# Performance work log

Hardware: AMD Instinct MI355X
Metric: run time of the kernel (lower is better)

## Reference

```python
import jax, jax.numpy as jnp
import numpy as np

CHUNK = 32  # chunk_size in _delta_rule_chunkwise

def _l2norm(x, eps=1e-6):
    return x * jax.lax.rsqrt(jnp.sum(x * x, axis=-1, keepdims=True) + eps)

def setup_inputs() -> dict:
    key = jax.random.key(0)
    kq, kk, kv, kb = jax.random.split(key, 4)
    b, h, L, dk, dv = 2, 8, 4096, 128, 128
    return {
        "q": jax.random.normal(kq, (b, h, L, dk), jnp.float32),
        "k": jax.random.normal(kk, (b, h, L, dk), jnp.float32),
        "v": jax.random.normal(kv, (b, h, L, dv), jnp.float32),
        "beta": jax.random.uniform(kb, (b, h, L), jnp.float32),  # sigmoid(b_proj) in (0,1)
    }

def _delta_rule_chunkwise(q, k, v, beta, chunk_size=CHUNK):
    b, h, L, dk = q.shape
    dv = v.shape[-1]
    c = chunk_size
    pad = (-L) % c
    if pad:
        q = jnp.pad(q, ((0, 0), (0, 0), (0, pad), (0, 0)))
        k = jnp.pad(k, ((0, 0), (0, 0), (0, pad), (0, 0)))
        v = jnp.pad(v, ((0, 0), (0, 0), (0, pad), (0, 0)))
        beta = jnp.pad(beta, ((0, 0), (0, 0), (0, pad)))
    n = (L + pad) // c
    q = _l2norm(q)
    k = _l2norm(k)
    v = v * beta[..., None]
    k_beta = k * beta[..., None]
    # [b,h,n,c,d]
    resh = lambda t: t.reshape(b, h, n, c, t.shape[-1])
    q, k, v, k_beta = map(resh, (q, k, v, k_beta))
    # strictly-lower-triangular -(k_beta k^T)
    lower = jnp.tril(jnp.ones((c, c), bool), -1)
    att = -(k_beta @ jnp.swapaxes(k, -1, -2)) * lower
    # forward substitution: invert (I - A) for strictly lower A (unrolled, c=32 static)
    for i in range(1, c):
        upd = jnp.einsum('...j,...jm->...m', att[..., i, :], att[..., :, :i])
        att = att.at[..., i, :i].add(upd)
    att = att + jnp.eye(c, dtype=att.dtype)
    att = att.astype(jnp.bfloat16).astype(q.dtype)  # matches .to(torch.bfloat16)
    u = att @ v         # [b,h,n,c,dv]
    w = att @ k_beta    # [b,h,n,c,dk]
    future = jnp.triu(jnp.ones((c, c), bool), 1)
    S0 = jnp.zeros((b, h, dk, dv), q.dtype)

    def step(S, inp):
        q_i, k_i, u_i, w_i = inp  # [b,h,c,d]
        att_local = jnp.where(future, 0.0, q_i @ jnp.swapaxes(k_i, -1, -2))
        u_new = u_i - w_i @ S
        o_i = q_i @ S + att_local @ u_new
        S_new = S + jnp.swapaxes(k_i, -1, -2) @ u_new
        return S_new, o_i

    xs = tuple(jnp.moveaxis(t, 2, 0) for t in (q, k, u, w))  # scan over chunks
    S, o = jax.lax.scan(step, S0, xs)
    o = jnp.moveaxis(o, 0, 2).reshape(b, h, n * c, dv)[:, :, :L]
    return o, S

def reference(q, k, v, beta):
    return _delta_rule_chunkwise(q, k, v, beta)
```

## Files before the change

kernel.cpp:

```cpp
#include <hip/hip_runtime.h>
#include <hip/hip_bf16.h>


#define B 2
#define H 8
#define LSEQ 4096
#define DK 128
#define DV 128
#define C 32
#define NCHUNK (LSEQ / C)
#define BH (B * H)
#define NBLK (BH * NCHUNK)
#define NG 16
#define GSZ 8

typedef _Float16 f16x8 __attribute__((ext_vector_type(8)));
typedef float f32x4 __attribute__((ext_vector_type(4)));

union U4H8 { uint4 u; f16x8 h; };

__device__ inline unsigned short f2h(float f) {
    _Float16 h = (_Float16)f;
    unsigned short u;
    __builtin_memcpy(&u, &h, 2);
    return u;
}
__device__ inline float h2f(unsigned int v) {
    unsigned short s = (unsigned short)v;
    _Float16 h;
    __builtin_memcpy(&h, &s, 2);
    return (float)h;
}
__device__ inline unsigned int pack2(float a, float b) {
    return (unsigned int)f2h(a) | ((unsigned int)f2h(b) << 16);
}
__device__ inline float dot4(float4 a, float4 b) {
    return a.x * b.x + a.y * b.y + a.z * b.z + a.w * b.w;
}
__device__ inline float bf16r(float x) {
    return __bfloat162float(__float2bfloat16(x));
}
__device__ inline uint2 pk4(float v0, float v1, float v2, float v3) {
    uint2 p; p.x = pack2(v0, v1); p.y = pack2(v2, v3); return p;
}
__device__ inline f32x4 up4(uint2 p) {
    f32x4 v;
    v[0] = h2f(p.x & 0xffffu); v[1] = h2f(p.x >> 16);
    v[2] = h2f(p.y & 0xffffu); v[3] = h2f(p.y >> 16);
    return v;
}

#define S40 40
#define S136 136

__global__ __launch_bounds__(64) void phase2_kernel(
    const float* __restrict__ qg, const float* __restrict__ kg,
    const float* __restrict__ vg, const float* __restrict__ betag,
    uint4* __restrict__ wnegf, uint4* __restrict__ qnf,
    uint4* __restrict__ ktf, uint4* __restrict__ atf,
    uint2* __restrict__ uf)
{
    __shared__ alignas(16) _Float16 sA [32 * S40];
    __shared__ alignas(16) _Float16 sAT[32 * S40];
    __shared__ alignas(16) _Float16 sTT[32 * S40];
    __shared__ alignas(16) _Float16 sTB[32 * S40];
    __shared__ alignas(16) _Float16 sW [32 * S136];
    __shared__ alignas(16) float sbetaL[32];
    __shared__ alignas(16) float skscL[32];

    const int l = threadIdx.x;
    const int lm = l & 15, qd = l >> 4;
    const int blk = blockIdx.x;
    const long tb = (long)blk * C * DK;
    const f32x4 z4 = {0.f, 0.f, 0.f, 0.f};

    if (l < 32) sbetaL[l] = betag[(long)blk * C + l];

    U4H8 qF[8], kF[8];
    float ssq[2] = {0.f, 0.f}, ssk[2] = {0.f, 0.f};
    #pragma unroll
    for (int mt = 0; mt < 2; mt++) {
        #pragma unroll
        for (int kt = 0; kt < 4; kt++) {
            const float* qp = qg + tb + (long)(mt * 16 + lm) * DK + kt * 32 + qd * 8;
            const float* kp = kg + tb + (long)(mt * 16 + lm) * DK + kt * 32 + qd * 8;
            float4 a0 = *(const float4*)qp, a1 = *(const float4*)(qp + 4);
            float4 b0 = *(const float4*)kp, b1 = *(const float4*)(kp + 4);
            ssq[mt] += dot4(a0, a0) + dot4(a1, a1);
            ssk[mt] += dot4(b0, b0) + dot4(b1, b1);
            U4H8 x;
            x.u.x = pack2(a0.x, a0.y); x.u.y = pack2(a0.z, a0.w);
            x.u.z = pack2(a1.x, a1.y); x.u.w = pack2(a1.z, a1.w);
            qF[mt * 4 + kt] = x;
            U4H8 y;
            y.u.x = pack2(b0.x, b0.y); y.u.y = pack2(b0.z, b0.w);
            y.u.z = pack2(b1.x, b1.y); y.u.w = pack2(b1.z, b1.w);
            kF[mt * 4 + kt] = y;
        }
    }
    float qsc[2], ksc[2];
    #pragma unroll
    for (int mt = 0; mt < 2; mt++) {
        float s = ssq[mt];
        s += __shfl_xor(s, 16, 64);
        s += __shfl_xor(s, 32, 64);
        qsc[mt] = rsqrtf(s + 1e-6f);
        float t = ssk[mt];
        t += __shfl_xor(t, 16, 64);
        t += __shfl_xor(t, 32, 64);
        ksc[mt] = rsqrtf(t + 1e-6f);
    }
    if (qd == 0) { skscL[lm] = ksc[0]; skscL[16 + lm] = ksc[1]; }

    f32x4 alT[3] = {z4, z4, z4};
    #pragma unroll
    for (int kt = 0; kt < 4; kt++) {
        alT[0] = __builtin_amdgcn_mfma_f32_16x16x32_f16(kF[kt].h,     qF[kt].h,     alT[0], 0, 0, 0);
        alT[1] = __builtin_amdgcn_mfma_f32_16x16x32_f16(kF[kt].h,     qF[4 + kt].h, alT[1], 0, 0, 0);
        alT[2] = __builtin_amdgcn_mfma_f32_16x16x32_f16(kF[4 + kt].h, qF[4 + kt].h, alT[2], 0, 0, 0);
    }
    #pragma unroll
    for (int mt = 0; mt < 2; mt++) {
        _Float16 qs = (_Float16)qsc[mt];
        #pragma unroll
        for (int kt = 0; kt < 4; kt++) {
            U4H8 x;
            x.h = qF[mt * 4 + kt].h * qs;
            qnf[((long)blk * 8 + mt * 4 + kt) * 64 + l] = x.u;
        }
    }
    f32x4 rw[4] = {z4, z4, z4, z4};
    #pragma unroll
    for (int kt = 0; kt < 4; kt++) {
        rw[0] = __builtin_amdgcn_mfma_f32_16x16x32_f16(kF[kt].h,     kF[kt].h,     rw[0], 0, 0, 0);
        rw[1] = __builtin_amdgcn_mfma_f32_16x16x32_f16(kF[kt].h,     kF[4 + kt].h, rw[1], 0, 0, 0);
        rw[2] = __builtin_amdgcn_mfma_f32_16x16x32_f16(kF[4 + kt].h, kF[kt].h,     rw[2], 0, 0, 0);
        rw[3] = __builtin_amdgcn_mfma_f32_16x16x32_f16(kF[4 + kt].h, kF[4 + kt].h, rw[3], 0, 0, 0);
    }

    float4 b4[2], ks4[2];
    b4[0]  = *(const float4*)&sbetaL[qd * 4];      b4[1]  = *(const float4*)&sbetaL[16 + qd * 4];
    ks4[0] = *(const float4*)&skscL[qd * 4];       ks4[1] = *(const float4*)&skscL[16 + qd * 4];
    const float bcol0 = sbetaL[lm], bcol1 = sbetaL[16 + lm];

    {
        *(uint2*)&sTB[lm * S40 + 16 + qd * 4] = (uint2){0u, 0u};
        float v[4];
        #pragma unroll
        for (int r = 0; r < 4; r++) {
            int c = qd * 4 + r;
            v[r] = (c <= lm) ? (qsc[0] * (&ks4[0].x)[r] * alT[0][r]) : 0.f;
        }
        *(uint2*)&sTB[lm * S40 + qd * 4] = pk4(v[0], v[1], v[2], v[3]);
        #pragma unroll
        for (int r = 0; r < 4; r++) v[r] = qsc[1] * (&ks4[0].x)[r] * alT[1][r];
        *(uint2*)&sTB[(16 + lm) * S40 + qd * 4] = pk4(v[0], v[1], v[2], v[3]);
        #pragma unroll
        for (int r = 0; r < 4; r++) {
            int c = qd * 4 + r;
            v[r] = (c <= lm) ? (qsc[1] * (&ks4[1].x)[r] * alT[2][r]) : 0.f;
        }
        *(uint2*)&sTB[(16 + lm) * S40 + 16 + qd * 4] = pk4(v[0], v[1], v[2], v[3]);
    }
    #pragma unroll
    for (int f = 0; f < 2; f++) {
        uint4 x = *(const uint4*)&sTB[(f * 16 + lm) * S40 + qd * 8];
        atf[((long)blk * 2 + f) * 64 + l] = x;
    }

    {
        float v[4];
        *(uint2*)&sA [lm * S40 + 16 + qd * 4]        = (uint2){0u, 0u};
        *(uint2*)&sAT[(16 + lm) * S40 + qd * 4]      = (uint2){0u, 0u};
        *(uint2*)&sTT[(16 + lm) * S40 + qd * 4]      = (uint2){0u, 0u};
        #pragma unroll
        for (int r = 0; r < 4; r++) {
            int c = qd * 4 + r;
            v[r] = (c < lm) ? (-bcol0 * ksc[0] * (&ks4[0].x)[r] * rw[0][r]) : 0.f;
        }
        *(uint2*)&sA[lm * S40 + qd * 4] = pk4(v[0], v[1], v[2], v[3]);
        #pragma unroll
        for (int r = 0; r < 4; r++) v[r] = -bcol1 * ksc[1] * (&ks4[0].x)[r] * rw[1][r];
        *(uint2*)&sA[(16 + lm) * S40 + qd * 4] = pk4(v[0], v[1], v[2], v[3]);
        #pragma unroll
        for (int r = 0; r < 4; r++) {
            int c = qd * 4 + r;
            v[r] = (c < lm) ? (-bcol1 * ksc[1] * (&ks4[1].x)[r] * rw[3][r]) : 0.f;
        }
        *(uint2*)&sA[(16 + lm) * S40 + 16 + qd * 4] = pk4(v[0], v[1], v[2], v[3]);
        #pragma unroll
        for (int r = 0; r < 4; r++) {
            int c = qd * 4 + r;
            v[r] = (c > lm) ? (-(&b4[0].x)[r] * (&ks4[0].x)[r] * ksc[0] * rw[0][r]) : 0.f;
        }
        *(uint2*)&sAT[lm * S40 + qd * 4] = pk4(v[0], v[1], v[2], v[3]);
        #pragma unroll
        for (int r = 0; r < 4; r++) v[r] = -(&b4[1].x)[r] * (&ks4[1].x)[r] * ksc[0] * rw[2][r];
        *(uint2*)&sAT[lm * S40 + 16 + qd * 4] = pk4(v[0], v[1], v[2], v[3]);
        #pragma unroll
        for (int r = 0; r < 4; r++) {
            int c = qd * 4 + r;
            v[r] = (c > lm) ? (-(&b4[1].x)[r] * (&ks4[1].x)[r] * ksc[1] * rw[3][r]) : 0.f;
        }
        *(uint2*)&sAT[(16 + lm) * S40 + 16 + qd * 4] = pk4(v[0], v[1], v[2], v[3]);
        #pragma unroll
        for (int r = 0; r < 4; r++) {
            int c = qd * 4 + r;
            v[r] = (c > lm) ? (-(&b4[0].x)[r] * (&ks4[0].x)[r] * ksc[0] * rw[0][r])
                            : ((c == lm) ? 1.0f : 0.f);
        }
        *(uint2*)&sTT[lm * S40 + qd * 4] = pk4(v[0], v[1], v[2], v[3]);
        #pragma unroll
        for (int r = 0; r < 4; r++) v[r] = -(&b4[1].x)[r] * (&ks4[1].x)[r] * ksc[0] * rw[2][r];
        *(uint2*)&sTT[lm * S40 + 16 + qd * 4] = pk4(v[0], v[1], v[2], v[3]);
        #pragma unroll
        for (int r = 0; r < 4; r++) {
            int c = qd * 4 + r;
            v[r] = (c > lm) ? (-(&b4[1].x)[r] * (&ks4[1].x)[r] * ksc[1] * rw[3][r])
                            : ((c == lm) ? 1.0f : 0.f);
        }
        *(uint2*)&sTT[(16 + lm) * S40 + 16 + qd * 4] = pk4(v[0], v[1], v[2], v[3]);
    }
    f32x4 Tc[3], TTc[3];
    #pragma unroll
    for (int r = 0; r < 4; r++) {
        int rr = qd * 4 + r;
        Tc[0][r] = (lm < rr) ? (-(&b4[0].x)[r] * (&ks4[0].x)[r] * ksc[0] * rw[0][r])
                             : ((lm == rr) ? 1.0f : 0.f);
        Tc[1][r] = -(&b4[1].x)[r] * (&ks4[1].x)[r] * ksc[0] * rw[2][r];
        Tc[2][r] = (lm < rr) ? (-(&b4[1].x)[r] * (&ks4[1].x)[r] * ksc[1] * rw[3][r])
                             : ((lm == rr) ? 1.0f : 0.f);
        TTc[0][r] = (rr < lm) ? (-bcol0 * ksc[0] * (&ks4[0].x)[r] * rw[0][r])
                              : ((rr == lm) ? 1.0f : 0.f);
        TTc[1][r] = -bcol1 * ksc[1] * (&ks4[0].x)[r] * rw[1][r];
        TTc[2][r] = (rr < lm) ? (-bcol1 * ksc[1] * (&ks4[1].x)[r] * rw[3][r])
                              : ((rr == lm) ? 1.0f : 0.f);
    }

    #pragma unroll
    for (int p = 0; p < 4; p++) {
        U4H8 AF[2], ATF[2], TTF[2];
        AF[0].u  = *(const uint4*)&sA [lm * S40 + qd * 8];
        AF[1].u  = *(const uint4*)&sA [(16 + lm) * S40 + qd * 8];
        ATF[0].u = *(const uint4*)&sAT[lm * S40 + qd * 8];
        ATF[1].u = *(const uint4*)&sAT[(16 + lm) * S40 + qd * 8];
        TTF[0].u = *(const uint4*)&sTT[lm * S40 + qd * 8];
        TTF[1].u = *(const uint4*)&sTT[(16 + lm) * S40 + qd * 8];

        f32x4 A2_00 = __builtin_amdgcn_mfma_f32_16x16x32_f16(AF[0].h, ATF[0].h, z4, 0, 0, 0);
        f32x4 A2_10 = __builtin_amdgcn_mfma_f32_16x16x32_f16(AF[1].h, ATF[0].h, z4, 0, 0, 0);
        f32x4 A2_11 = __builtin_amdgcn_mfma_f32_16x16x32_f16(AF[1].h, ATF[1].h, z4, 0, 0, 0);
        f32x4 A2T_00 = __builtin_amdgcn_mfma_f32_16x16x32_f16(ATF[0].h, AF[0].h, z4, 0, 0, 0);
        f32x4 A2T_01 = __builtin_amdgcn_mfma_f32_16x16x32_f16(ATF[0].h, AF[1].h, z4, 0, 0, 0);
        f32x4 A2T_11 = __builtin_amdgcn_mfma_f32_16x16x32_f16(ATF[1].h, AF[1].h, z4, 0, 0, 0);

        {
            float v[4];
            #pragma unroll
            for (int r = 0; r < 4; r++) { int c = qd * 4 + r; v[r] = (c < lm) ? A2T_00[r] : 0.f; }
            *(uint2*)&sA[lm * S40 + qd * 4] = pk4(v[0], v[1], v[2], v[3]);
            *(uint2*)&sA[(16 + lm) * S40 + qd * 4] = pk4(A2T_01[0], A2T_01[1], A2T_01[2], A2T_01[3]);
            #pragma unroll
            for (int r = 0; r < 4; r++) { int c = qd * 4 + r; v[r] = (c < lm) ? A2T_11[r] : 0.f; }
            *(uint2*)&sA[(16 + lm) * S40 + 16 + qd * 4] = pk4(v[0], v[1], v[2], v[3]);
        }
        if (p < 3) {
            float v[4];
            #pragma unroll
            for (int r = 0; r < 4; r++) { int c = qd * 4 + r; v[r] = (c > lm) ? A2_00[r] : 0.f; }
            *(uint2*)&sAT[lm * S40 + qd * 4] = pk4(v[0], v[1], v[2], v[3]);
            *(uint2*)&sAT[lm * S40 + 16 + qd * 4] = pk4(A2_10[0], A2_10[1], A2_10[2], A2_10[3]);
            #pragma unroll
            for (int r = 0; r < 4; r++) { int c = qd * 4 + r; v[r] = (c > lm) ? A2_11[r] : 0.f; }
            *(uint2*)&sAT[(16 + lm) * S40 + 16 + qd * 4] = pk4(v[0], v[1], v[2], v[3]);
        }
        U4H8 AnF[2];
        AnF[0].u = *(const uint4*)&sA[lm * S40 + qd * 8];
        AnF[1].u = *(const uint4*)&sA[(16 + lm) * S40 + qd * 8];
        Tc[0]  = __builtin_amdgcn_mfma_f32_16x16x32_f16(AnF[0].h, TTF[0].h, Tc[0], 0, 0, 0);
        Tc[1]  = __builtin_amdgcn_mfma_f32_16x16x32_f16(AnF[1].h, TTF[0].h, Tc[1], 0, 0, 0);
        Tc[2]  = __builtin_amdgcn_mfma_f32_16x16x32_f16(AnF[1].h, TTF[1].h, Tc[2], 0, 0, 0);
        TTc[0] = __builtin_amdgcn_mfma_f32_16x16x32_f16(TTF[0].h, AnF[0].h, TTc[0], 0, 0, 0);
        TTc[1] = __builtin_amdgcn_mfma_f32_16x16x32_f16(TTF[0].h, AnF[1].h, TTc[1], 0, 0, 0);
        TTc[2] = __builtin_amdgcn_mfma_f32_16x16x32_f16(TTF[1].h, AnF[1].h, TTc[2], 0, 0, 0);
        if (p < 3) {
            *(uint2*)&sTT[lm * S40 + qd * 4]             = pk4(Tc[0][0], Tc[0][1], Tc[0][2], Tc[0][3]);
            *(uint2*)&sTT[lm * S40 + 16 + qd * 4]        = pk4(Tc[1][0], Tc[1][1], Tc[1][2], Tc[1][3]);
            *(uint2*)&sTT[(16 + lm) * S40 + 16 + qd * 4] = pk4(Tc[2][0], Tc[2][1], Tc[2][2], Tc[2][3]);
        }
    }

    {
        *(uint2*)&sTB[lm * S40 + 16 + qd * 4] = (uint2){0u, 0u};
        float v[4];
        #pragma unroll
        for (int r = 0; r < 4; r++) v[r] = bf16r(TTc[0][r]) * (&b4[0].x)[r];
        *(uint2*)&sTB[lm * S40 + qd * 4] = pk4(v[0], v[1], v[2], v[3]);
        #pragma unroll
        for (int r = 0; r < 4; r++) v[r] = bf16r(TTc[1][r]) * (&b4[0].x)[r];
        *(uint2*)&sTB[(16 + lm) * S40 + qd * 4] = pk4(v[0], v[1], v[2], v[3]);
        #pragma unroll
        for (int r = 0; r < 4; r++) v[r] = bf16r(TTc[2][r]) * (&b4[1].x)[r];
        *(uint2*)&sTB[(16 + lm) * S40 + 16 + qd * 4] = pk4(v[0], v[1], v[2], v[3]);
    }
    U4H8 TbF[2];
    TbF[0].u = *(const uint4*)&sTB[lm * S40 + qd * 8];
    TbF[1].u = *(const uint4*)&sTB[(16 + lm) * S40 + qd * 8];

    float kscj[8];
    #pragma unroll
    for (int j = 0; j < 8; j++) kscj[j] = skscL[qd * 8 + j];
    #pragma unroll
    for (int nt = 0; nt < 8; nt++) {
        U4H8 bV, bK;
        #pragma unroll
        for (int j = 0; j < 8; j++) {
            const long ro = tb + (long)(qd * 8 + j) * DK + nt * 16 + lm;
            bV.h[j] = (_Float16)vg[ro];
            bK.h[j] = (_Float16)(kg[ro] * kscj[j]);
        }
        ktf[((long)blk * 8 + nt) * 64 + l] = bK.u;
        f32x4 u0 = __builtin_amdgcn_mfma_f32_16x16x32_f16(TbF[0].h, bV.h, z4, 0, 0, 0);
        f32x4 u1 = __builtin_amdgcn_mfma_f32_16x16x32_f16(TbF[1].h, bV.h, z4, 0, 0, 0);
        uf[(((long)blk * 2 + 0) * 8 + nt) * 64 + l] = pk4(u0[0], u0[1], u0[2], u0[3]);
        uf[(((long)blk * 2 + 1) * 8 + nt) * 64 + l] = pk4(u1[0], u1[1], u1[2], u1[3]);
        f32x4 w0 = __builtin_amdgcn_mfma_f32_16x16x32_f16(TbF[0].h, bK.h, z4, 0, 0, 0);
        f32x4 w1 = __builtin_amdgcn_mfma_f32_16x16x32_f16(TbF[1].h, bK.h, z4, 0, 0, 0);
        #pragma unroll
        for (int r = 0; r < 4; r++) {
            sW[(qd * 4 + r) * S136 + nt * 16 + lm]        = (_Float16)(-w0[r]);
            sW[(16 + qd * 4 + r) * S136 + nt * 16 + lm]   = (_Float16)(-w1[r]);
        }
    }
    #pragma unroll
    for (int mt2 = 0; mt2 < 2; mt2++) {
        #pragma unroll
        for (int kt = 0; kt < 4; kt++) {
            uint4 x = *(const uint4*)&sW[(mt2 * 16 + lm) * S136 + kt * 32 + qd * 8];
            wnegf[((long)blk * 8 + mt2 * 4 + kt) * 64 + l] = x;
        }
    }
}

__global__ __launch_bounds__(64, 2) void phase3a_kernel(
    const uint4* __restrict__ wnegf, const uint4* __restrict__ ktf,
    const uint2* __restrict__ uf,
    uint4* __restrict__ Pf, uint2* __restrict__ Qgf)
{
    __shared__ alignas(16) _Float16 S16[16 * 16 * 8];
    __shared__ alignas(16) _Float16 U16[4 * 16 * 8];
    __shared__ alignas(16) _Float16 PT[128 * 16];

    const int l = threadIdx.x;
    const int lm = l & 15, quad = l >> 4;
    const int idx = blockIdx.x;
    const int s = idx >> 8;
    const int g = idx & 255;
    const int mode = s >> 3;
    const int w = s & 7;
    const int bh = g >> 4;
    const int grp = g & 15;
    const f32x4 z4 = {0.f, 0.f, 0.f, 0.f};

    if (mode && grp == 0) return;

    f32x4 accS[8];
    #pragma unroll
    for (int mt = 0; mt < 8; mt++) {
        #pragma unroll
        for (int r = 0; r < 4; r++)
            accS[mt][r] = (mode && mt == w && quad * 4 + r == lm) ? 1.f : 0.f;
    }

    struct FragA { uint4 aW[2][4]; uint4 aK[8]; uint2 aU[2]; };
    FragA fA, fB;

    auto loadf = [&](FragA& f, int t) {
        const long blk = (long)bh * NCHUNK + grp * GSZ + t;
        #pragma unroll
        for (int mt2 = 0; mt2 < 2; mt2++)
            #pragma unroll
            for (int kt = 0; kt < 4; kt++)
                f.aW[mt2][kt] = wnegf[(blk * 8 + mt2 * 4 + kt) * 64 + l];
        #pragma unroll
        for (int mt = 0; mt < 8; mt++) f.aK[mt] = ktf[(blk * 8 + mt) * 64 + l];
        if (!mode) {
            #pragma unroll
            for (int mt2 = 0; mt2 < 2; mt2++)
                f.aU[mt2] = uf[((blk * 2 + mt2) * 8 + w) * 64 + l];
        }
    };

    auto compute = [&](const FragA& f) {
        #pragma unroll
        for (int mt = 0; mt < 8; mt++) {
            int g2 = 2 * mt + (quad >> 1);
            int sub = (quad & 1) * 4;
            *(uint2*)&S16[(g2 * 16 + lm) * 8 + sub] =
                pk4(accS[mt][0], accS[mt][1], accS[mt][2], accS[mt][3]);
        }
        f32x4 accU[2];
        #pragma unroll
        for (int mt2 = 0; mt2 < 2; mt2++)
            accU[mt2] = mode ? z4 : up4(f.aU[mt2]);
        #pragma unroll
        for (int kt = 0; kt < 4; kt++) {
            U4H8 bs;
            bs.u = *(const uint4*)&S16[((kt * 4 + quad) * 16 + lm) * 8];
            #pragma unroll
            for (int mt2 = 0; mt2 < 2; mt2++) {
                U4H8 aw; aw.u = f.aW[mt2][kt];
                accU[mt2] = __builtin_amdgcn_mfma_f32_16x16x32_f16(aw.h, bs.h, accU[mt2], 0, 0, 0);
            }
        }
        #pragma unroll
        for (int mt2 = 0; mt2 < 2; mt2++) {
            int g2 = 2 * mt2 + (quad >> 1);
            int sub = (quad & 1) * 4;
            *(uint2*)&U16[(g2 * 16 + lm) * 8 + sub] =
                pk4(accU[mt2][0], accU[mt2][1], accU[mt2][2], accU[mt2][3]);
        }
        U4H8 bu;
        bu.u = *(const uint4*)&U16[(quad * 16 + lm) * 8];
        #pragma unroll
        for (int mt = 0; mt < 8; mt++) {
            U4H8 ak; ak.u = f.aK[mt];
            accS[mt] = __builtin_amdgcn_mfma_f32_16x16x32_f16(ak.h, bu.h, accS[mt], 0, 0, 0);
        }
    };

    loadf(fA, 0);
    #pragma unroll 1
    for (int t = 0; t < GSZ; t += 2) {
        loadf(fB, t + 1);
        compute(fA);
        if (t + 2 < GSZ) loadf(fA, t + 2);
        compute(fB);
    }

    if (!mode) {
        const long qb = (((long)(bh * NG + grp)) * 8 + w) * 8 * 64;
        #pragma unroll
        for (int mt = 0; mt < 8; mt++)
            Qgf[qb + mt * 64 + l] = pk4(accS[mt][0], accS[mt][1], accS[mt][2], accS[mt][3]);
    } else {
        #pragma unroll
        for (int mt = 0; mt < 8; mt++)
            #pragma unroll
            for (int r = 0; r < 4; r++)
                PT[(mt * 16 + quad * 4 + r) * 16 + lm] = (_Float16)accS[mt][r];
        const int tl = ((w & 1) << 5) | (l & 31);
        const int half = l >> 5;
        const long pb = ((long)(bh * NG + grp)) * 8;
        #pragma unroll
        for (int i = 0; i < 4; i++) {
            int mt = half * 4 + i;
            uint4 x = *(const uint4*)&PT[(mt * 16 + (tl & 15)) * 16 + ((tl >> 4) & 1) * 8];
            Pf[((pb + mt) * 4 + (w >> 1)) * 64 + tl] = x;
        }
    }
}

__global__ __launch_bounds__(64, 1) void phase3b_kernel(
    const uint4* __restrict__ Pf, const uint2* __restrict__ Qgf,
    uint2* __restrict__ Sjf, float* __restrict__ S_out)
{
    __shared__ alignas(16) _Float16 S16[16 * 16 * 8];

    const int l = threadIdx.x;
    const int lm = l & 15, quad = l >> 4;
    const int bh = blockIdx.x & 15;
    const int w = blockIdx.x >> 4;

    f32x4 accS[8];
    #pragma unroll
    for (int mt = 0; mt < 8; mt++) accS[mt] = (f32x4){0.f, 0.f, 0.f, 0.f};

    uint2 Q0[8], Q1[8];
    uint4 P0[8][4], P1[8][4];

    auto loadQ = [&](uint2 (&Q)[8], int j) {
        const long b = (((long)(bh * NG + j)) * 8 + w) * 8 * 64;
        #pragma unroll
        for (int mt = 0; mt < 8; mt++) Q[mt] = Qgf[b + mt * 64 + l];
    };
    auto loadP = [&](uint4 (&P)[8][4], int j) {
        const long b = ((long)(bh * NG + j)) * 8;
        #pragma unroll
        for (int mt = 0; mt < 8; mt++)
            #pragma unroll
            for (int kt = 0; kt < 4; kt++)
                P[mt][kt] = Pf[((b + mt) * 4 + kt) * 64 + l];
    };
    auto computeB = [&](int j, const uint2 (&Q)[8], const uint4 (&P)[8][4]) {
        f32x4 ns[8];
        #pragma unroll
        for (int mt = 0; mt < 8; mt++) ns[mt] = up4(Q[mt]);
        if (j) {
            #pragma unroll
            for (int mt = 0; mt < 8; mt++) {
                int g2 = 2 * mt + (quad >> 1);
                int sub = (quad & 1) * 4;
                *(uint2*)&S16[(g2 * 16 + lm) * 8 + sub] =
                    pk4(accS[mt][0], accS[mt][1], accS[mt][2], accS[mt][3]);
            }
            #pragma unroll
            for (int kt = 0; kt < 4; kt++) {
                U4H8 bs;
                bs.u = *(const uint4*)&S16[((kt * 4 + quad) * 16 + lm) * 8];
                #pragma unroll
                for (int mt = 0; mt < 8; mt++) {
                    U4H8 ap; ap.u = P[mt][kt];
                    ns[mt] = __builtin_amdgcn_mfma_f32_16x16x32_f16(ap.h, bs.h, ns[mt], 0, 0, 0);
                }
            }
        }
        #pragma unroll
        for (int mt = 0; mt < 8; mt++) accS[mt] = ns[mt];
        if (j < 15) {
            const long sb = (((long)(bh * 16 + (j + 1))) * 8 + w) * 8 * 64;
            #pragma unroll
            for (int mt = 0; mt < 8; mt++)
                Sjf[sb + mt * 64 + l] = pk4(ns[mt][0], ns[mt][1], ns[mt][2], ns[mt][3]);
        } else {
            #pragma unroll
            for (int mt = 0; mt < 8; mt++)
                #pragma unroll
                for (int r = 0; r < 4; r++)
                    S_out[(long)bh * (DK * DV) + (long)(mt * 16 + quad * 4 + r) * DV + w * 16 + lm] = ns[mt][r];
        }
    };

    loadQ(Q0, 0);
    loadP(P1, 1);
    #pragma unroll 1
    for (int j = 0; j < 16; j += 2) {
        loadQ(Q1, j + 1);
        computeB(j, Q0, P0);
        if (j + 2 < 16) { loadP(P0, j + 2); loadQ(Q0, j + 2); }
        computeB(j + 1, Q1, P1);
        if (j + 3 < 16) loadP(P1, j + 3);
    }
}

struct Frags {
    uint4 aW[2][4];
    uint4 aQ[2][4];
    uint4 aK[8];
    uint4 aAt[2];
    uint2 aU[2];
};

__global__ __launch_bounds__(64, 1) void phase3c_kernel(
    const uint4* __restrict__ wnegf, const uint4* __restrict__ qnf,
    const uint4* __restrict__ ktf, const uint4* __restrict__ atf,
    const uint2* __restrict__ uf, const uint2* __restrict__ Sjf,
    float* __restrict__ o_out)
{
    __shared__ alignas(16) _Float16 S16[16 * 16 * 8];
    __shared__ alignas(16) _Float16 U16[4 * 16 * 8];

    const int l = threadIdx.x;
    const int lm = l & 15, quad = l >> 4;
    const int idx = blockIdx.x;
    const int w = idx >> 8;
    const int g = idx & 255;
    const int bh = g >> 4;
    const int grp = g & 15;
    const int dv = w * 16 + lm;

    f32x4 accS[8];
    if (grp == 0) {
        #pragma unroll
        for (int mt = 0; mt < 8; mt++) accS[mt] = (f32x4){0.f, 0.f, 0.f, 0.f};
    } else {
        const long sb = (((long)(bh * 16 + grp)) * 8 + w) * 8 * 64;
        #pragma unroll
        for (int mt = 0; mt < 8; mt++) accS[mt] = up4(Sjf[sb + mt * 64 + l]);
    }

    auto loadf = [&](Frags& f, int t) {
        const long blk = (long)bh * NCHUNK + grp * GSZ + t;
        #pragma unroll
        for (int mt2 = 0; mt2 < 2; mt2++) {
            #pragma unroll
            for (int kt = 0; kt < 4; kt++) {
                f.aW[mt2][kt] = wnegf[(blk * 8 + mt2 * 4 + kt) * 64 + l];
                f.aQ[mt2][kt] = qnf[(blk * 8 + mt2 * 4 + kt) * 64 + l];
            }
            f.aAt[mt2] = atf[(blk * 2 + mt2) * 64 + l];
            f.aU[mt2] = uf[((blk * 2 + mt2) * 8 + w) * 64 + l];
        }
        #pragma unroll
        for (int mt = 0; mt < 8; mt++) f.aK[mt] = ktf[(blk * 8 + mt) * 64 + l];
    };

    auto compute = [&](const Frags& f, int t) {
        #pragma unroll
        for (int mt = 0; mt < 8; mt++) {
            int g2 = 2 * mt + (quad >> 1);
            int sub = (quad & 1) * 4;
            *(uint2*)&S16[(g2 * 16 + lm) * 8 + sub] =
                pk4(accS[mt][0], accS[mt][1], accS[mt][2], accS[mt][3]);
        }
        f32x4 accU[2], accO[2];
        #pragma unroll
        for (int mt2 = 0; mt2 < 2; mt2++) {
            accU[mt2] = up4(f.aU[mt2]);
            accO[mt2] = (f32x4){0.f, 0.f, 0.f, 0.f};
        }
        #pragma unroll
        for (int kt = 0; kt < 4; kt++) {
            U4H8 bs;
            bs.u = *(const uint4*)&S16[((kt * 4 + quad) * 16 + lm) * 8];
            #pragma unroll
            for (int mt2 = 0; mt2 < 2; mt2++) {
                U4H8 aw, aq;
                aw.u = f.aW[mt2][kt];
                aq.u = f.aQ[mt2][kt];
                accU[mt2] = __builtin_amdgcn_mfma_f32_16x16x32_f16(aw.h, bs.h, accU[mt2], 0, 0, 0);
                accO[mt2] = __builtin_amdgcn_mfma_f32_16x16x32_f16(aq.h, bs.h, accO[mt2], 0, 0, 0);
            }
        }
        #pragma unroll
        for (int mt2 = 0; mt2 < 2; mt2++) {
            int g2 = 2 * mt2 + (quad >> 1);
            int sub = (quad & 1) * 4;
            *(uint2*)&U16[(g2 * 16 + lm) * 8 + sub] =
                pk4(accU[mt2][0], accU[mt2][1], accU[mt2][2], accU[mt2][3]);
        }
        U4H8 bu;
        bu.u = *(const uint4*)&U16[(quad * 16 + lm) * 8];
        const long ob = ((long)bh * LSEQ + (long)(grp * GSZ + t) * C) * DV;
        #pragma unroll
        for (int mt2 = 0; mt2 < 2; mt2++) {
            U4H8 aa;
            aa.u = f.aAt[mt2];
            accO[mt2] = __builtin_amdgcn_mfma_f32_16x16x32_f16(aa.h, bu.h, accO[mt2], 0, 0, 0);
            #pragma unroll
            for (int r = 0; r < 4; r++)
                o_out[ob + (long)(mt2 * 16 + quad * 4 + r) * DV + dv] = accO[mt2][r];
        }
        #pragma unroll
        for (int mt = 0; mt < 8; mt++) {
            U4H8 ak;
            ak.u = f.aK[mt];
            accS[mt] = __builtin_amdgcn_mfma_f32_16x16x32_f16(ak.h, bu.h, accS[mt], 0, 0, 0);
        }
    };

    Frags fA, fB;
    loadf(fA, 0);
    #pragma unroll 1
    for (int t = 0; t < GSZ; t += 2) {
        loadf(fB, t + 1);
        compute(fA, t);
        if (t + 2 < GSZ) loadf(fA, t + 2);
        compute(fB, t + 1);
    }
}

extern "C" void kernel_launch(void* const* d_in, const int* in_sizes, int n_in,
                              void* d_out, int out_size, void* d_ws, size_t ws_size,
                              hipStream_t stream) {
    const float* q    = (const float*)d_in[0];
    const float* k    = (const float*)d_in[1];
    const float* v    = (const float*)d_in[2];
    const float* beta = (const float*)d_in[3];

    float* o = (float*)d_out;
    float* S = o + (long)BH * LSEQ * DV;

    const size_t nwq = (size_t)NBLK * 8 * 64;
    uint4* wnegf = (uint4*)d_ws;
    uint4* qnf = wnegf + nwq;
    uint4* ktf = qnf + nwq;
    uint4* atf = ktf + nwq;
    uint2* uf  = (uint2*)(atf + (size_t)NBLK * 2 * 64);
    uint4* Pf  = (uint4*)(uf + (size_t)NBLK * 16 * 64);
    uint2* Qgf = (uint2*)(Pf + (size_t)BH * NG * 8 * 4 * 64);
    uint2* Sjf = Qgf + (size_t)BH * NG * 8 * 8 * 64;

    phase2_kernel<<<NBLK, 64, 0, stream>>>(q, k, v, beta, wnegf, qnf, ktf, atf, uf);
    phase3a_kernel<<<16 * 256, 64, 0, stream>>>(wnegf, ktf, uf, Pf, Qgf);
    phase3b_kernel<<<BH * 8, 64, 0, stream>>>(Pf, Qgf, Sjf, S);
    phase3c_kernel<<<8 * 256, 64, 0, stream>>>(wnegf, qnf, ktf, atf, uf, Sjf, o);
}
```

Baseline: 222.6 us.

## Split phase3b sequential state scan across four wavefronts per block

The phase3b kernel, which runs the sequential inter-group state recurrence with only 128 single-wave blocks, now uses 256 threads per block. Each of the four waves owns two of the eight row tiles. The state is shared through a double-buffered LDS tile, with a block barrier before the MFMA reads. This shortens each wave's serial MFMA and load chain on the latency-bound critical path, at the cost of one __syncthreads per step.

```diff
diff --git a/kernel.cpp b/kernel.cpp
--- a/kernel.cpp
+++ b/kernel.cpp
@@ -461,73 +461,80 @@
     }
 }
 
-__global__ __launch_bounds__(64, 1) void phase3b_kernel(
+__global__ __launch_bounds__(256, 1) void phase3b_kernel(
     const uint4* __restrict__ Pf, const uint2* __restrict__ Qgf,
     uint2* __restrict__ Sjf, float* __restrict__ S_out)
 {
-    __shared__ alignas(16) _Float16 S16[16 * 16 * 8];
-
-    const int l = threadIdx.x;
+    __shared__ alignas(16) _Float16 S16[2][16 * 16 * 8];
+
+    const int tid = threadIdx.x;
+    const int l = tid & 63;
+    const int ww = tid >> 6;
     const int lm = l & 15, quad = l >> 4;
     const int bh = blockIdx.x & 15;
     const int w = blockIdx.x >> 4;
 
-    f32x4 accS[8];
-    #pragma unroll
-    for (int mt = 0; mt < 8; mt++) accS[mt] = (f32x4){0.f, 0.f, 0.f, 0.f};
-
-    uint2 Q0[8], Q1[8];
-    uint4 P0[8][4], P1[8][4];
-
-    auto loadQ = [&](uint2 (&Q)[8], int j) {
+    f32x4 accS[2];
+    #pragma unroll
+    for (int i = 0; i < 2; i++) accS[i] = (f32x4){0.f, 0.f, 0.f, 0.f};
+
+    uint2 Q0[2], Q1[2];
+    uint4 P0[2][4], P1[2][4];
+
+    auto loadQ = [&](uint2 (&Q)[2], int j) {
         const long b = (((long)(bh * NG + j)) * 8 + w) * 8 * 64;
         #pragma unroll
-        for (int mt = 0; mt < 8; mt++) Q[mt] = Qgf[b + mt * 64 + l];
+        for (int i = 0; i < 2; i++) Q[i] = Qgf[b + (ww * 2 + i) * 64 + l];
     };
-    auto loadP = [&](uint4 (&P)[8][4], int j) {
+    auto loadP = [&](uint4 (&P)[2][4], int j) {
         const long b = ((long)(bh * NG + j)) * 8;
         #pragma unroll
-        for (int mt = 0; mt < 8; mt++)
+        for (int i = 0; i < 2; i++)
             #pragma unroll
             for (int kt = 0; kt < 4; kt++)
-                P[mt][kt] = Pf[((b + mt) * 4 + kt) * 64 + l];
+                P[i][kt] = Pf[((b + ww * 2 + i) * 4 + kt) * 64 + l];
     };
-    auto computeB = [&](int j, const uint2 (&Q)[8], const uint4 (&P)[8][4]) {
-        f32x4 ns[8];
-        #pragma unroll
-        for (int mt = 0; mt < 8; mt++) ns[mt] = up4(Q[mt]);
+    auto computeB = [&](int j, const uint2 (&Q)[2], const uint4 (&P)[2][4]) {
+        f32x4 ns[2];
+        #pragma unroll
+        for (int i = 0; i < 2; i++) ns[i] = up4(Q[i]);
         if (j) {
-            #pragma unroll
-            for (int mt = 0; mt < 8; mt++) {
+            const int buf = j & 1;
+            #pragma unroll
+            for (int i = 0; i < 2; i++) {
+                int mt = ww * 2 + i;
                 int g2 = 2 * mt + (quad >> 1);
                 int sub = (quad & 1) * 4;
-                *(uint2*)&S16[(g2 * 16 + lm) * 8 + sub] =
-                    pk4(accS[mt][0], accS[mt][1], accS[mt][2], accS[mt][3]);
+                *(uint2*)&S16[buf][(g2 * 16 + lm) * 8 + sub] =
+                    pk4(accS[i][0], accS[i][1], accS[i][2], accS[i][3]);
             }
+            __syncthreads();
             #pragma unroll
             for (int kt = 0; kt < 4; kt++) {
                 U4H8 bs;
-                bs.u = *(const uint4*)&S16[((kt * 4 + quad) * 16 + lm) * 8];
+                bs.u = *(const uint4*)&S16[buf][((kt * 4 + quad) * 16 + lm) * 8];
                 #pragma unroll
-                for (int mt = 0; mt < 8; mt++) {
-                    U4H8 ap; ap.u = P[mt][kt];
-                    ns[mt] = __builtin_amdgcn_mfma_f32_16x16x32_f16(ap.h, bs.h, ns[mt], 0, 0, 0);
+                for (int i = 0; i < 2; i++) {
+                    U4H8 ap; ap.u = P[i][kt];
+                    ns[i] = __builtin_amdgcn_mfma_f32_16x16x32_f16(ap.h, bs.h, ns[i], 0, 0, 0);
                 }
             }
         }
         #pragma unroll
-        for (int mt = 0; mt < 8; mt++) accS[mt] = ns[mt];
+        for (int i = 0; i < 2; i++) accS[i] = ns[i];
         if (j < 15) {
             const long sb = (((long)(bh * 16 + (j + 1))) * 8 + w) * 8 * 64;
             #pragma unroll
-            for (int mt = 0; mt < 8; mt++)
-                Sjf[sb + mt * 64 + l] = pk4(ns[mt][0], ns[mt][1], ns[mt][2], ns[mt][3]);
+            for (int i = 0; i < 2; i++)
+                Sjf[sb + (ww * 2 + i) * 64 + l] = pk4(ns[i][0], ns[i][1], ns[i][2], ns[i][3]);
         } else {
             #pragma unroll
-            for (int mt = 0; mt < 8; mt++)
+            for (int i = 0; i < 2; i++) {
+                int mt = ww * 2 + i;
                 #pragma unroll
                 for (int r = 0; r < 4; r++)
-                    S_out[(long)bh * (DK * DV) + (long)(mt * 16 + quad * 4 + r) * DV + w * 16 + lm] = ns[mt][r];
+                    S_out[(long)bh * (DK * DV) + (long)(mt * 16 + quad * 4 + r) * DV + w * 16 + lm] = ns[i][r];
+            }
         }
     };
 
@@ -683,6 +690,6 @@
 
     phase2_kernel<<<NBLK, 64, 0, stream>>>(q, k, v, beta, wnegf, qnf, ktf, atf, uf);
     phase3a_kernel<<<16 * 256, 64, 0, stream>>>(wnegf, ktf, uf, Pf, Qgf);
-    phase3b_kernel<<<BH * 8, 64, 0, stream>>>(Pf, Qgf, Sjf, S);
+    phase3b_kernel<<<BH * 8, 256, 0, stream>>>(Pf, Qgf, Sjf, S);
     phase3c_kernel<<<8 * 256, 64, 0, stream>>>(wnegf, qnf, ktf, atf, uf, Sjf, o);
 }
```

After: 217.5 us. -2.3%, faster.
